# Optimization experiments

Hardware: AMD Instinct MI355X
Metric: run time of the kernel (lower is better)

Reference implementation:

```python
import jax, jax.numpy as jnp
import numpy as np

N_WORD, N_TOPIC, N_DOC = 30000, 512, 10000
E_WT, E_WD, E_TD = 262144, 262144, 131072
D_IN, D_OUT = 256, 256


def _mean_agg(msg, dst, n):
    # scatter-mean: sum of messages / in-degree (0 for isolated nodes via max(deg,1))
    s = jax.ops.segment_sum(msg, dst, num_segments=n)
    deg = jax.ops.segment_sum(jnp.ones((msg.shape[0],), msg.dtype), dst, num_segments=n)
    return s / jnp.maximum(deg, 1.0)[:, None]


def setup_inputs() -> dict:
    key = jax.random.key(0)
    ks = jax.random.split(key, 16)
    inp = {
        "feat_word": jax.random.normal(ks[0], (N_WORD, D_IN), jnp.float32),
        "feat_topic": jax.random.normal(ks[1], (N_TOPIC, D_IN), jnp.float32),
        "feat_doc": jax.random.normal(ks[2], (N_DOC, D_IN), jnp.float32),
        "wt_src": jax.random.randint(ks[3], (E_WT,), 0, N_WORD, jnp.int32),
        "wt_dst": jax.random.randint(ks[4], (E_WT,), 0, N_TOPIC, jnp.int32),
        "wd_src": jax.random.randint(ks[5], (E_WD,), 0, N_WORD, jnp.int32),
        "wd_dst": jax.random.randint(ks[6], (E_WD,), 0, N_DOC, jnp.int32),
        "td_src": jax.random.randint(ks[7], (E_TD,), 0, N_TOPIC, jnp.int32),
        "td_dst": jax.random.randint(ks[8], (E_TD,), 0, N_DOC, jnp.int32),
        "w_wt": jax.random.uniform(ks[9], (E_WT,), jnp.float32),
        "w_wd": jax.random.uniform(ks[10], (E_WD,), jnp.float32),
        "w_td": jax.random.uniform(ks[11], (E_TD,), jnp.float32),
        # per-relation Linear params (torch convention: W [out,in], y = x @ W.T + b)
        "Wt": jax.random.normal(ks[12], (D_OUT, D_IN), jnp.float32) * 0.02,
        "bt": jnp.zeros((D_OUT,), jnp.float32),
        "Wd": jax.random.normal(ks[13], (D_OUT, D_IN), jnp.float32) * 0.02,
        "bd": jnp.zeros((D_OUT,), jnp.float32),
        "Wtd": jax.random.normal(ks[14], (D_OUT, D_IN), jnp.float32) * 0.02,
        "btd": jnp.zeros((D_OUT,), jnp.float32),
    }
    return inp


def reference(feat_word, feat_topic, feat_doc,
              wt_src, wt_dst, wd_src, wd_dst, td_src, td_dst,
              w_wt, w_wd, w_td,
              Wt, bt, Wd, bd, Wtd, btd):
    # per-relation Linear on source node features (computed once per src node)
    Wh_wt = feat_word @ Wt.T + bt    # [N_WORD, D_OUT]
    Wh_wd = feat_word @ Wd.T + bd    # [N_WORD, D_OUT]
    Wh_td = feat_topic @ Wtd.T + btd  # [N_TOPIC, D_OUT]

    # u_mul_e then mean per destination
    h_topic = _mean_agg(Wh_wt[wt_src] * w_wt[:, None], wt_dst, N_TOPIC)
    m_wd = _mean_agg(Wh_wd[wd_src] * w_wd[:, None], wd_dst, N_DOC)
    m_td = _mean_agg(Wh_td[td_src] * w_td[:, None], td_dst, N_DOC)

    # cross-type reducer 'sum'; doc nodes get activation (dropout is eval/identity)
    h_doc = jax.nn.relu(m_wd + m_td)

    # word nodes receive no messages: their 'h' stays the input features
    return feat_word, h_topic, h_doc
```

## Files before the change

### kernel.cpp

```cpp
#include <hip/hip_runtime.h>
#include <hip/hip_bf16.h>

#define N_WORD  30000
#define N_TOPIC 512
#define N_DOC   10000
#define E_WT    262144
#define E_WD    262144
#define E_TD    131072
#define DIM     256
#define WT_BINS 16
#define SB_WT   (N_TOPIC * WT_BINS)
#define CAP_WT  96
#define CAP_WD  72
#define CAP_TD  48
#define CSTRIDE 16

typedef __attribute__((ext_vector_type(8))) short bf16x8;
typedef __attribute__((ext_vector_type(4))) float f32x4;
typedef __attribute__((ext_vector_type(2))) int int2v;
typedef __attribute__((ext_vector_type(4))) int int4v;

__device__ __forceinline__ short f2bf(float f) {
    __hip_bfloat16 h = __float2bfloat16(f);
    short s;
    __builtin_memcpy(&s, &h, 2);
    return s;
}
__device__ __forceinline__ void acc8(float* a, int4v d, float w) {
    #pragma unroll
    for (int k = 0; k < 4; ++k) {
        union { unsigned int u; float f; } lo, hi;
        lo.u = ((unsigned int)d[k]) << 16;
        hi.u = ((unsigned int)d[k]) & 0xffff0000u;
        a[2 * k]     += lo.f * w;
        a[2 * k + 1] += hi.f * w;
    }
}

#define WT_SBLK 256
#define WD_SBLK 256
#define TD_SBLK 128
#define SCATTER_BLOCKS (WT_SBLK + WD_SBLK + TD_SBLK)
#define FWCAST_BLOCKS 3750
#define FTCAST_BLOCKS 64
#define WCAST_BLOCKS  96
#define SC_BLOCKS (SCATTER_BLOCKS + FWCAST_BLOCKS + FTCAST_BLOCKS + WCAST_BLOCKS)

__global__ __launch_bounds__(256) void scatter_cast(
    const int* __restrict__ wt_src, const int* __restrict__ wt_dst, const float* __restrict__ w_wt,
    const int* __restrict__ wd_src, const int* __restrict__ wd_dst, const float* __restrict__ w_wd,
    const int* __restrict__ td_src, const int* __restrict__ td_dst, const float* __restrict__ w_td,
    int* __restrict__ cur_wt, int* __restrict__ cur_wd, int* __restrict__ cur_td,
    int2v* __restrict__ pk_wt, int2v* __restrict__ pk_wd, int2v* __restrict__ pk_td,
    const float* __restrict__ feat_word, const float* __restrict__ feat_topic,
    const float* __restrict__ Wt, const float* __restrict__ Wd, const float* __restrict__ Wtd,
    __hip_bfloat16* __restrict__ fw, __hip_bfloat16* __restrict__ ft,
    __hip_bfloat16* __restrict__ wbt, __hip_bfloat16* __restrict__ wbd,
    __hip_bfloat16* __restrict__ wbtd)
{
    int b = blockIdx.x;
    if (b < WT_SBLK) {
        int e0 = b * 1024 + (int)threadIdx.x;
        int s[4], sb[4], pos[4];
        float wv[4];
        #pragma unroll
        for (int k = 0; k < 4; ++k) {
            int e = e0 + k * 256;
            s[k] = wt_src[e];
            sb[k] = wt_dst[e] * WT_BINS + (s[k] >> 11);
            wv[k] = w_wt[e];
        }
        #pragma unroll
        for (int k = 0; k < 4; ++k) pos[k] = atomicAdd(&cur_wt[sb[k] * CSTRIDE], 1);
        #pragma unroll
        for (int k = 0; k < 4; ++k)
            if (pos[k] < CAP_WT) {
                int2v p; p.x = s[k]; p.y = __float_as_int(wv[k]);
                pk_wt[(size_t)sb[k] * CAP_WT + pos[k]] = p;
            }
        return;
    }
    if (b < WT_SBLK + WD_SBLK) {
        int e0 = (b - WT_SBLK) * 1024 + (int)threadIdx.x;
        int s[4], d[4], pos[4];
        float wv[4];
        #pragma unroll
        for (int k = 0; k < 4; ++k) {
            int e = e0 + k * 256;
            s[k] = wd_src[e];
            d[k] = wd_dst[e];
            wv[k] = w_wd[e];
        }
        #pragma unroll
        for (int k = 0; k < 4; ++k) pos[k] = atomicAdd(&cur_wd[d[k] * CSTRIDE], 1);
        #pragma unroll
        for (int k = 0; k < 4; ++k)
            if (pos[k] < CAP_WD) {
                int2v p; p.x = s[k]; p.y = __float_as_int(wv[k]);
                pk_wd[(size_t)d[k] * CAP_WD + pos[k]] = p;
            }
        return;
    }
    if (b < SCATTER_BLOCKS) {
        int e0 = (b - WT_SBLK - WD_SBLK) * 1024 + (int)threadIdx.x;
        int s[4], d[4], pos[4];
        float wv[4];
        #pragma unroll
        for (int k = 0; k < 4; ++k) {
            int e = e0 + k * 256;
            s[k] = td_src[e];
            d[k] = td_dst[e];
            wv[k] = w_td[e];
        }
        #pragma unroll
        for (int k = 0; k < 4; ++k) pos[k] = atomicAdd(&cur_td[d[k] * CSTRIDE], 1);
        #pragma unroll
        for (int k = 0; k < 4; ++k)
            if (pos[k] < CAP_TD) {
                int2v p; p.x = s[k]; p.y = __float_as_int(wv[k]);
                pk_td[(size_t)d[k] * CAP_TD + pos[k]] = p;
            }
        return;
    }
    const float* src;
    unsigned short* dst;
    int local;
    int cb = b - SCATTER_BLOCKS;
    if (cb < FWCAST_BLOCKS) { src = feat_word; local = cb * 256 + (int)threadIdx.x; dst = (unsigned short*)fw; }
    else if (cb < FWCAST_BLOCKS + FTCAST_BLOCKS) {
        src = feat_topic; local = (cb - FWCAST_BLOCKS) * 256 + (int)threadIdx.x; dst = (unsigned short*)ft;
    } else {
        int i = (cb - FWCAST_BLOCKS - FTCAST_BLOCKS) * 256 + (int)threadIdx.x;
        if (i < 8192) { src = Wt; local = i; dst = (unsigned short*)wbt; }
        else if (i < 16384) { src = Wd; local = i - 8192; dst = (unsigned short*)wbd; }
        else { src = Wtd; local = i - 16384; dst = (unsigned short*)wbtd; }
    }
    f32x4 a = *reinterpret_cast<const f32x4*>(src + (size_t)local * 8);
    f32x4 c = *reinterpret_cast<const f32x4*>(src + (size_t)local * 8 + 4);
    bf16x8 r;
    r[0] = f2bf(a[0]); r[1] = f2bf(a[1]); r[2] = f2bf(a[2]); r[3] = f2bf(a[3]);
    r[4] = f2bf(c[0]); r[5] = f2bf(c[1]); r[6] = f2bf(c[2]); r[7] = f2bf(c[3]);
    *reinterpret_cast<bf16x8*>(dst + (size_t)local * 8) = r;
}

#define GATHER_BLOCKS (SB_WT / 4 + 2 * N_DOC / 4)
#define COPY_BLOCKS 3750
#define GC_BLOCKS (GATHER_BLOCKS + COPY_BLOCKS)
__global__ __launch_bounds__(256) void gather_all(
    const __hip_bfloat16* __restrict__ fw, const __hip_bfloat16* __restrict__ ft,
    const int2v* __restrict__ pk_wt, const int* __restrict__ cur_wt,
    const int2v* __restrict__ pk_wd, const int* __restrict__ cur_wd,
    const int2v* __restrict__ pk_td, const int* __restrict__ cur_td,
    float* __restrict__ part, float* __restrict__ part_sumw,
    __hip_bfloat16* __restrict__ agg_wd, float* __restrict__ mw_wd,
    __hip_bfloat16* __restrict__ agg_td, float* __restrict__ mw_td,
    const float* __restrict__ feat_word, float* __restrict__ out_word)
{
    int bb = blockIdx.x;
    int wv = threadIdx.x >> 6;
    int lane = threadIdx.x & 63;
    int l = lane & 31, hi = lane >> 5;

    if (bb >= GATHER_BLOCKS) {
        int i = (bb - GATHER_BLOCKS) * 256 + (int)threadIdx.x;
        f32x4 a = *reinterpret_cast<const f32x4*>(feat_word + (size_t)i * 8);
        f32x4 c = *reinterpret_cast<const f32x4*>(feat_word + (size_t)i * 8 + 4);
        *reinterpret_cast<f32x4*>(out_word + (size_t)i * 8) = a;
        *reinterpret_cast<f32x4*>(out_word + (size_t)i * 8 + 4) = c;
        return;
    }

    const int2v* pk;
    const unsigned short* T;
    int cnt, deg = 0;
    bool is_wt = bb < SB_WT / 4;
    int node, chunk = 0;
    __hip_bfloat16* agg = nullptr;
    float* mw = nullptr;

    if (is_wt) {
        int xcd = bb & 7;
        int idx = bb >> 3;
        chunk = (idx & 1) * 8 + xcd;
        node = (idx >> 1) * 4 + wv;
        int base = node * WT_BINS + chunk;
        cnt = cur_wt[base * CSTRIDE]; if (cnt > CAP_WT) cnt = CAP_WT;
        pk = pk_wt + (size_t)base * CAP_WT;
        T = (const unsigned short*)fw;
    } else {
        int w2 = (bb - SB_WT / 4) * 4 + wv;
        int rel = w2 >= N_DOC;
        node = rel ? w2 - N_DOC : w2;
        T = (const unsigned short*)(rel ? ft : fw);
        const int2v* pkb = rel ? pk_td : pk_wd;
        const int* cur = rel ? cur_td : cur_wd;
        const int cap = rel ? CAP_TD : CAP_WD;
        agg = rel ? agg_td : agg_wd;
        mw = rel ? mw_td : mw_wd;
        deg = cur[node * CSTRIDE];
        cnt = deg > cap ? cap : deg;
        pk = pkb + (size_t)node * cap;
    }

    float acc[8] = {0.f, 0.f, 0.f, 0.f, 0.f, 0.f, 0.f, 0.f};
    float sw = 0.f;
    int j = 0;
    for (; j + 8 <= cnt; j += 8) {
        int2v p[8];
        #pragma unroll
        for (int k = 0; k < 8; ++k) p[k] = pk[j + k];
        int4v v[4];
        #pragma unroll
        for (int q = 0; q < 4; ++q) {
            int r = hi ? p[2 * q + 1].x : p[2 * q].x;
            v[q] = *reinterpret_cast<const int4v*>(T + (size_t)r * DIM + l * 8);
        }
        #pragma unroll
        for (int q = 0; q < 4; ++q) {
            float w = __int_as_float(hi ? p[2 * q + 1].y : p[2 * q].y);
            acc8(acc, v[q], w);
            sw += w;
        }
    }
    for (; j + 2 <= cnt; j += 2) {
        int2v p0 = pk[j], p1 = pk[j + 1];
        int r = hi ? p1.x : p0.x;
        float w = __int_as_float(hi ? p1.y : p0.y);
        int4v v = *reinterpret_cast<const int4v*>(T + (size_t)r * DIM + l * 8);
        acc8(acc, v, w);
        sw += w;
    }
    if (j < cnt) {
        int2v p0 = pk[j];
        float w = hi ? 0.f : __int_as_float(p0.y);
        int4v v = *reinterpret_cast<const int4v*>(T + (size_t)p0.x * DIM + l * 8);
        acc8(acc, v, w);
        sw += w;
    }
    #pragma unroll
    for (int k = 0; k < 8; ++k) acc[k] += __shfl_xor(acc[k], 32, 64);
    sw += __shfl_xor(sw, 32, 64);

    if (is_wt) {
        if (hi == 0) {
            float* pdst = part + ((size_t)chunk * N_TOPIC + node) * DIM + l * 8;
            f32x4 r0 = {acc[0], acc[1], acc[2], acc[3]};
            f32x4 r1 = {acc[4], acc[5], acc[6], acc[7]};
            *reinterpret_cast<f32x4*>(pdst) = r0;
            *reinterpret_cast<f32x4*>(pdst + 4) = r1;
        }
        if (lane == 0) part_sumw[chunk * N_TOPIC + node] = sw;
    } else {
        float inv = 1.f / (float)(deg > 1 ? deg : 1);
        if (hi == 0) {
            int4v r;
            #pragma unroll
            for (int k = 0; k < 4; ++k) {
                unsigned int lo = (unsigned short)f2bf(acc[2 * k] * inv);
                unsigned int hb = (unsigned short)f2bf(acc[2 * k + 1] * inv);
                r[k] = (int)((hb << 16) | lo);
            }
            *reinterpret_cast<int4v*>((unsigned short*)agg + (size_t)node * DIM + l * 8) = r;
        }
        if (lane == 0) mw[node] = sw * inv;
    }
}

#define DOC_STRIPS 625
#define STRIPS_PER_XCD 79
#define DOC_BLOCKS (8 * STRIPS_PER_XCD * 4)
#define GEMM_BLOCKS (32 + DOC_BLOCKS)

__global__ __launch_bounds__(256, 1) void gemm_all(
    const float* __restrict__ part, const float* __restrict__ part_sumw,
    const int* __restrict__ cur_wt,
    const __hip_bfloat16* __restrict__ wbt, const float* __restrict__ bt,
    const __hip_bfloat16* __restrict__ agg_wd, const __hip_bfloat16* __restrict__ wbd,
    const float* __restrict__ bd, const float* __restrict__ mw_d1,
    const __hip_bfloat16* __restrict__ agg_td, const __hip_bfloat16* __restrict__ wbtd,
    const float* __restrict__ btd, const float* __restrict__ mw_d2,
    float* __restrict__ out_topic, float* __restrict__ out_doc)
{
    int lane = threadIdx.x & 63;
    int wv = threadIdx.x >> 6;
    int lr = lane & 15, kh = lane >> 4;

    if (blockIdx.x < 32) {
        __shared__ unsigned short A[16][DIM + 8];
        __shared__ float mwv[16];
        __shared__ float invv[16];
        int rt = blockIdx.x;
        int t = threadIdx.x;
        if (t < 16) {
            int node = rt * 16 + t;
            int d = 0;
            float swt = 0.f;
            #pragma unroll
            for (int c = 0; c < WT_BINS; ++c) {
                int v = cur_wt[(node * WT_BINS + c) * CSTRIDE];
                d += v > CAP_WT ? CAP_WT : v;
                swt += part_sumw[c * N_TOPIC + node];
            }
            float inv = 1.f / (float)(d > 1 ? d : 1);
            invv[t] = inv;
            mwv[t] = swt * inv;
        }
        __syncthreads();
        for (int i = t; i < 16 * DIM; i += 256) {
            int n = i >> 8, d = i & 255;
            int node = rt * 16 + n;
            float s = 0.f;
            #pragma unroll
            for (int c = 0; c < WT_BINS; ++c)
                s += part[((size_t)c * N_TOPIC + node) * DIM + d];
            A[n][d] = (unsigned short)f2bf(s * invv[n]);
        }
        __syncthreads();
        #pragma unroll
        for (int q = 0; q < 4; ++q) {
            int ct = wv * 4 + q;
            f32x4 acc = {0.f, 0.f, 0.f, 0.f};
            const unsigned short* Ab = &A[lr][kh * 8];
            const unsigned short* Wb = (const unsigned short*)wbt + (size_t)(ct * 16 + lr) * DIM + kh * 8;
            #pragma unroll
            for (int kk = 0; kk < 8; ++kk) {
                bf16x8 a = *reinterpret_cast<const bf16x8*>(Ab + kk * 32);
                bf16x8 b = *reinterpret_cast<const bf16x8*>(Wb + kk * 32);
                acc = __builtin_amdgcn_mfma_f32_16x16x32_bf16(a, b, acc, 0, 0, 0);
            }
            float bb = bt[ct * 16 + lr];
            #pragma unroll
            for (int j = 0; j < 4; ++j) {
                int n = kh * 4 + j;
                out_topic[(size_t)(rt * 16 + n) * DIM + ct * 16 + lr] = acc[j] + bb * mwv[n];
            }
        }
        return;
    }

    int b = blockIdx.x - 32;
    int xcd = b & 7;
    int idx = b >> 3;
    int rt = xcd * STRIPS_PER_XCD + (idx >> 2);
    if (rt >= DOC_STRIPS) return;
    int ct = (idx & 3) * 4 + wv;

    const unsigned short* A1 = (const unsigned short*)agg_wd + (size_t)(rt * 16 + lr) * DIM + kh * 8;
    const unsigned short* A2 = (const unsigned short*)agg_td + (size_t)(rt * 16 + lr) * DIM + kh * 8;
    const unsigned short* W1 = (const unsigned short*)wbd  + (size_t)(ct * 16 + lr) * DIM + kh * 8;
    const unsigned short* W2 = (const unsigned short*)wbtd + (size_t)(ct * 16 + lr) * DIM + kh * 8;

    bf16x8 a1[8], a2[8], w1[8], w2[8];
    #pragma unroll
    for (int kk = 0; kk < 8; ++kk) {
        a1[kk] = *reinterpret_cast<const bf16x8*>(A1 + kk * 32);
        a2[kk] = *reinterpret_cast<const bf16x8*>(A2 + kk * 32);
        w1[kk] = *reinterpret_cast<const bf16x8*>(W1 + kk * 32);
        w2[kk] = *reinterpret_cast<const bf16x8*>(W2 + kk * 32);
    }
    f32x4 acc = {0.f, 0.f, 0.f, 0.f};
    #pragma unroll
    for (int kk = 0; kk < 8; ++kk)
        acc = __builtin_amdgcn_mfma_f32_16x16x32_bf16(a1[kk], w1[kk], acc, 0, 0, 0);
    #pragma unroll
    for (int kk = 0; kk < 8; ++kk)
        acc = __builtin_amdgcn_mfma_f32_16x16x32_bf16(a2[kk], w2[kk], acc, 0, 0, 0);

    float bb1 = bd[ct * 16 + lr];
    float bb2 = btd[ct * 16 + lr];
    #pragma unroll
    for (int j = 0; j < 4; ++j) {
        int row = rt * 16 + kh * 4 + j;
        float v = acc[j] + bb1 * mw_d1[row] + bb2 * mw_d2[row];
        out_doc[(size_t)row * DIM + ct * 16 + lr] = fmaxf(v, 0.f);
    }
}

extern "C" void kernel_launch(void* const* d_in, const int* in_sizes, int n_in,
                              void* d_out, int out_size, void* d_ws, size_t ws_size,
                              hipStream_t stream)
{
    const float* feat_word  = (const float*)d_in[0];
    const float* feat_topic = (const float*)d_in[1];
    const int* wt_src = (const int*)d_in[3];
    const int* wt_dst = (const int*)d_in[4];
    const int* wd_src = (const int*)d_in[5];
    const int* wd_dst = (const int*)d_in[6];
    const int* td_src = (const int*)d_in[7];
    const int* td_dst = (const int*)d_in[8];
    const float* w_wt = (const float*)d_in[9];
    const float* w_wd = (const float*)d_in[10];
    const float* w_td = (const float*)d_in[11];
    const float* Wt   = (const float*)d_in[12];
    const float* bt   = (const float*)d_in[13];
    const float* Wd   = (const float*)d_in[14];
    const float* bd   = (const float*)d_in[15];
    const float* Wtd  = (const float*)d_in[16];
    const float* btd  = (const float*)d_in[17];

    char* ws = (char*)d_ws;
    __hip_bfloat16* fw     = (__hip_bfloat16*)(ws + 0);
    __hip_bfloat16* ft     = (__hip_bfloat16*)(ws + 15360000);
    __hip_bfloat16* wbt    = (__hip_bfloat16*)(ws + 15622144);
    __hip_bfloat16* wbd    = (__hip_bfloat16*)(ws + 15753216);
    __hip_bfloat16* wbtd   = (__hip_bfloat16*)(ws + 15884288);
    __hip_bfloat16* agg_wd = (__hip_bfloat16*)(ws + 16015360);
    __hip_bfloat16* agg_td = (__hip_bfloat16*)(ws + 21135360);
    float* part      = (float*)(ws + 26255360);
    float* part_sumw = (float*)(ws + 34643968);
    float* mw_wd     = (float*)(ws + 34676736);
    float* mw_td     = (float*)(ws + 34716736);
    int* cur_wt = (int*)(ws + 34756736);
    int* cur_wd = (int*)(ws + 35281024);
    int* cur_td = (int*)(ws + 35921024);
    int2v* pk_wt = (int2v*)(ws + 36561024);
    int2v* pk_wd = (int2v*)(ws + 42852480);
    int2v* pk_td = (int2v*)(ws + 48612480);

    float* out = (float*)d_out;
    float* out_topic = out + (size_t)N_WORD * DIM;
    float* out_doc   = out + (size_t)(N_WORD + N_TOPIC) * DIM;

    hipMemsetAsync(ws + 34756736, 0, 1804288, stream);

    scatter_cast<<<SC_BLOCKS, 256, 0, stream>>>(
        wt_src, wt_dst, w_wt, wd_src, wd_dst, w_wd, td_src, td_dst, w_td,
        cur_wt, cur_wd, cur_td, pk_wt, pk_wd, pk_td,
        feat_word, feat_topic, Wt, Wd, Wtd, fw, ft, wbt, wbd, wbtd);

    gather_all<<<GC_BLOCKS, 256, 0, stream>>>(
        fw, ft,
        pk_wt, cur_wt,
        pk_wd, cur_wd,
        pk_td, cur_td,
        part, part_sumw, agg_wd, mw_wd, agg_td, mw_td,
        feat_word, out);

    gemm_all<<<GEMM_BLOCKS, 256, 0, stream>>>(
        part, part_sumw, cur_wt,
        wbt, bt,
        agg_wd, wbd, bd, mw_wd,
        agg_td, wbtd, btd, mw_td,
        out_topic, out_doc);
}
```

Measured before the change: 128.0 us.

## Tile doc GEMM as 32-row blocks with LDS-staged aggregates covering all columns

The doc-node GEMM previously used 16x64 tiles (4 waves, one column tile each), so each block re-read A rows from global memory across four blocks per strip, and the grid was XCD-swizzled. Each block now stages 32 rows of both aggregated relations into shared memory once and loops over all 16 column tiles (4 per wave). This cuts redundant A traffic and reduces the block count to 313. In exchange, each wave reloads weight fragments per column tile, the work per block is serialized, and the grid loses its XCD-aware mapping. The launch bound no longer forces one block per CU, which allows higher occupancy despite the larger LDS footprint.

```diff
diff --git a/kernel.cpp b/kernel.cpp
--- a/kernel.cpp
+++ b/kernel.cpp
@@ -266,12 +266,11 @@
     }
 }
 
-#define DOC_STRIPS 625
-#define STRIPS_PER_XCD 79
-#define DOC_BLOCKS (8 * STRIPS_PER_XCD * 4)
+#define DOC_BLOCKS 313
 #define GEMM_BLOCKS (32 + DOC_BLOCKS)
-
-__global__ __launch_bounds__(256, 1) void gemm_all(
+#define LROW (DIM + 8)
+
+__global__ __launch_bounds__(256) void gemm_all(
     const float* __restrict__ part, const float* __restrict__ part_sumw,
     const int* __restrict__ cur_wt,
     const __hip_bfloat16* __restrict__ wbt, const float* __restrict__ bt,
@@ -284,13 +283,13 @@
     int lane = threadIdx.x & 63;
     int wv = threadIdx.x >> 6;
     int lr = lane & 15, kh = lane >> 4;
+    int t = threadIdx.x;
 
     if (blockIdx.x < 32) {
-        __shared__ unsigned short A[16][DIM + 8];
+        __shared__ unsigned short A[16][LROW];
         __shared__ float mwv[16];
         __shared__ float invv[16];
         int rt = blockIdx.x;
-        int t = threadIdx.x;
         if (t < 16) {
             int node = rt * 16 + t;
             int d = 0;
@@ -338,41 +337,69 @@
         return;
     }
 
+    __shared__ unsigned short As[2][32][LROW];
     int b = blockIdx.x - 32;
-    int xcd = b & 7;
-    int idx = b >> 3;
-    int rt = xcd * STRIPS_PER_XCD + (idx >> 2);
-    if (rt >= DOC_STRIPS) return;
-    int ct = (idx & 3) * 4 + wv;
-
-    const unsigned short* A1 = (const unsigned short*)agg_wd + (size_t)(rt * 16 + lr) * DIM + kh * 8;
-    const unsigned short* A2 = (const unsigned short*)agg_td + (size_t)(rt * 16 + lr) * DIM + kh * 8;
-    const unsigned short* W1 = (const unsigned short*)wbd  + (size_t)(ct * 16 + lr) * DIM + kh * 8;
-    const unsigned short* W2 = (const unsigned short*)wbtd + (size_t)(ct * 16 + lr) * DIM + kh * 8;
-
-    bf16x8 a1[8], a2[8], w1[8], w2[8];
+    int rb = b * 32;
+    int nrows = N_DOC - rb; if (nrows > 32) nrows = 32;
+
+    if (nrows == 32) {
+        for (int i = t; i < 2 * 32 * 32; i += 256) {
+            int rel = i >> 10;
+            int rem = i & 1023;
+            int row = rem >> 5;
+            int c8 = rem & 31;
+            const unsigned short* src =
+                (const unsigned short*)(rel ? agg_td : agg_wd) + (size_t)(rb + row) * DIM + c8 * 8;
+            *reinterpret_cast<bf16x8*>(&As[rel][row][c8 * 8]) =
+                *reinterpret_cast<const bf16x8*>(src);
+        }
+    } else {
+        for (int i = t; i < 2 * nrows * 32; i += 256) {
+            int rel = i / (nrows * 32);
+            int rem = i % (nrows * 32);
+            int row = rem >> 5;
+            int c8 = rem & 31;
+            const unsigned short* src =
+                (const unsigned short*)(rel ? agg_td : agg_wd) + (size_t)(rb + row) * DIM + c8 * 8;
+            *reinterpret_cast<bf16x8*>(&As[rel][row][c8 * 8]) =
+                *reinterpret_cast<const bf16x8*>(src);
+        }
+    }
+    __syncthreads();
+
+    int nsub = nrows >> 4;
     #pragma unroll
-    for (int kk = 0; kk < 8; ++kk) {
-        a1[kk] = *reinterpret_cast<const bf16x8*>(A1 + kk * 32);
-        a2[kk] = *reinterpret_cast<const bf16x8*>(A2 + kk * 32);
-        w1[kk] = *reinterpret_cast<const bf16x8*>(W1 + kk * 32);
-        w2[kk] = *reinterpret_cast<const bf16x8*>(W2 + kk * 32);
-    }
-    f32x4 acc = {0.f, 0.f, 0.f, 0.f};
-    #pragma unroll
-    for (int kk = 0; kk < 8; ++kk)
-        acc = __builtin_amdgcn_mfma_f32_16x16x32_bf16(a1[kk], w1[kk], acc, 0, 0, 0);
-    #pragma unroll
-    for (int kk = 0; kk < 8; ++kk)
-        acc = __builtin_amdgcn_mfma_f32_16x16x32_bf16(a2[kk], w2[kk], acc, 0, 0, 0);
-
-    float bb1 = bd[ct * 16 + lr];
-    float bb2 = btd[ct * 16 + lr];
-    #pragma unroll
-    for (int j = 0; j < 4; ++j) {
-        int row = rt * 16 + kh * 4 + j;
-        float v = acc[j] + bb1 * mw_d1[row] + bb2 * mw_d2[row];
-        out_doc[(size_t)row * DIM + ct * 16 + lr] = fmaxf(v, 0.f);
+    for (int q = 0; q < 4; ++q) {
+        int ct = wv * 4 + q;
+        const unsigned short* W1 = (const unsigned short*)wbd  + (size_t)(ct * 16 + lr) * DIM + kh * 8;
+        const unsigned short* W2 = (const unsigned short*)wbtd + (size_t)(ct * 16 + lr) * DIM + kh * 8;
+        bf16x8 w1[8], w2[8];
+        #pragma unroll
+        for (int kk = 0; kk < 8; ++kk) {
+            w1[kk] = *reinterpret_cast<const bf16x8*>(W1 + kk * 32);
+            w2[kk] = *reinterpret_cast<const bf16x8*>(W2 + kk * 32);
+        }
+        float bb1 = bd[ct * 16 + lr];
+        float bb2 = btd[ct * 16 + lr];
+        for (int sub = 0; sub < nsub; ++sub) {
+            f32x4 acc = {0.f, 0.f, 0.f, 0.f};
+            const unsigned short* A1 = &As[0][sub * 16 + lr][kh * 8];
+            const unsigned short* A2 = &As[1][sub * 16 + lr][kh * 8];
+            #pragma unroll
+            for (int kk = 0; kk < 8; ++kk)
+                acc = __builtin_amdgcn_mfma_f32_16x16x32_bf16(
+                    *reinterpret_cast<const bf16x8*>(A1 + kk * 32), w1[kk], acc, 0, 0, 0);
+            #pragma unroll
+            for (int kk = 0; kk < 8; ++kk)
+                acc = __builtin_amdgcn_mfma_f32_16x16x32_bf16(
+                    *reinterpret_cast<const bf16x8*>(A2 + kk * 32), w2[kk], acc, 0, 0, 0);
+            #pragma unroll
+            for (int j = 0; j < 4; ++j) {
+                int row = rb + sub * 16 + kh * 4 + j;
+                float v = acc[j] + bb1 * mw_d1[row] + bb2 * mw_d2[row];
+                out_doc[(size_t)row * DIM + ct * 16 + lr] = fmaxf(v, 0.f);
+            }
+        }
     }
 }
 
```

Result: faster. 108.9 us (-14.9%).
